# Kernel optimization log

Measured on AMD Instinct MI355X. Metric: run time of the kernel, lower is better.

## Reference

```python
import jax, jax.numpy as jnp
import numpy as np

N_NODES = 100000
N_EDGES = 1600000
IN_DIM = 256
OUT_DIM = 128


def setup_inputs() -> dict:
    key = jax.random.key(0)
    k1, k2, k3, k4, k5 = jax.random.split(key, 5)
    h = jax.random.normal(k1, (N_NODES, IN_DIM), dtype=jnp.float32)
    # xavier_normal-ish scales for the two weight matrices
    W = jax.random.normal(k2, (IN_DIM, OUT_DIM), dtype=jnp.float32) * (2.0 / np.sqrt(IN_DIM + OUT_DIM))
    a = jax.random.normal(k3, (2 * OUT_DIM,), dtype=jnp.float32) * (2.0 / np.sqrt(2 * OUT_DIM + 1))
    src = jax.random.randint(k4, (N_EDGES,), 0, N_NODES, dtype=jnp.int32)
    dst = jax.random.randint(k5, (N_EDGES,), 0, N_NODES, dtype=jnp.int32)
    return {"h": h, "W": W, "a": a, "src": src, "dst": dst}


def reference(h, W, a, src, dst):
    n = h.shape[0]
    d = W.shape[1]
    z = h @ W  # [N, out_dim]
    # attn_fc([z_src || z_dst]) == z_src @ a[:d] + z_dst @ a[d:]
    el = z @ a[:d]  # [N]
    er = z @ a[d:]  # [N]
    e = jax.nn.leaky_relu(el[src] + er[dst])  # [E], torch default slope 0.01
    # per-destination (segment) softmax, numerically stable
    seg_max = jax.ops.segment_max(e, dst, num_segments=n)
    e_exp = jnp.exp(e - seg_max[dst])
    denom = jax.ops.segment_sum(e_exp, dst, num_segments=n)
    alpha = e_exp / denom[dst]  # [E]
    # weighted scatter-sum of source z into destinations
    h_out = jax.ops.segment_sum(alpha[:, None] * z[src], dst, num_segments=n)
    return h_out
```

## Files before the change

### kernel.cpp

```cpp
#include <hip/hip_runtime.h>
#include <cstdint>
#include <cstddef>

#define N_NODES 100000
#define N_EDGES 1600000
#define IN_DIM  256
#define OUT_DIM 128

#define BSHIFT 7
#define BNODES 128
#define NBUCK  782
#define BCAP   3200
#define CNTMAX 2816
#define MAXE   6
#define EPB    2048
#define PB     782
#define GBP    1564

typedef __attribute__((ext_vector_type(8))) short bf16x8;
typedef __attribute__((ext_vector_type(4))) float f32x4;

__device__ __forceinline__ unsigned bf16rn(float f) {
    unsigned u = __float_as_uint(f);
    return (u + 0x7FFFu + ((u >> 16) & 1u)) >> 16;
}

__global__ __launch_bounds__(256) void setup_k(
    const float* __restrict__ W, unsigned short* __restrict__ w16s,
    int* __restrict__ bucket_cursor)
{
    int t = blockIdx.x * blockDim.x + threadIdx.x;
    if (t < NBUCK) bucket_cursor[t] = 0;
    if (t >= IN_DIM * OUT_DIM) return;
    int j  = t & 7;
    int n  = (t >> 3) & 15;
    int q  = (t >> 7) & 3;
    int c  = (t >> 9) & 7;
    int kc = t >> 12;
    int k   = kc * 32 + q * 8 + j;
    int dim = (c >> 1) * 32 + n * 2 + (c & 1);
    w16s[t] = (unsigned short)bf16rn(W[k * OUT_DIM + dim]);
}

__global__ __launch_bounds__(256, 3) void pg_k(
    const int* __restrict__ src, const int* __restrict__ dst,
    int* __restrict__ bucket_cursor, unsigned* __restrict__ ebuf,
    const float* __restrict__ h, const unsigned short* __restrict__ w16s,
    const float* __restrict__ a,
    unsigned short* __restrict__ z16, float* __restrict__ el, float* __restrict__ er)
{
    __shared__ int hist[NBUCK];
    __shared__ int gbaseL[NBUCK];
    const int t   = threadIdx.x;
    const int bid = blockIdx.x;

    if ((bid % 3) == 2) {
        const int pid = bid / 3;
        for (int i = t; i < NBUCK; i += 256) hist[i] = 0;
        __syncthreads();

        const int e0 = pid * EPB;
        int bucks[8], ranks[8];
        unsigned pk[8];
        #pragma unroll
        for (int k = 0; k < 8; ++k) {
            int e = e0 + k * 256 + t;
            bucks[k] = -1;
            if (e < N_EDGES) {
                int s = src[e], d = dst[e];
                int b = d >> BSHIFT;
                bucks[k] = b;
                ranks[k] = atomicAdd(&hist[b], 1);
                pk[k] = ((unsigned)s << BSHIFT) | (unsigned)(d & (BNODES - 1));
            }
        }
        __syncthreads();
        for (int i = t; i < NBUCK; i += 256) {
            int hc = hist[i];
            gbaseL[i] = hc ? atomicAdd(&bucket_cursor[i], hc) : 0;
        }
        __syncthreads();
        #pragma unroll
        for (int k = 0; k < 8; ++k)
            if (bucks[k] >= 0) {
                int p = gbaseL[bucks[k]] + ranks[k];
                if (p < BCAP)
                    ebuf[(size_t)bucks[k] * BCAP + p] = pk[k];
            }
        return;
    }

    const int gid  = (bid / 3) * 2 + (bid % 3);
    const int n0   = gid * 64;
    const int w    = t >> 6;
    const int lane = t & 63;
    const int q    = lane >> 4;
    const int col  = lane & 15;

    int row  = n0 + w * 16 + col;
    int lrow = (row < N_NODES) ? row : (N_NODES - 1);
    const float* hp = h + (size_t)lrow * IN_DIM + q * 8;

    float4 va[16];
    #pragma unroll
    for (int kc = 0; kc < 8; ++kc) {
        va[2 * kc]     = *(const float4*)(hp + kc * 32);
        va[2 * kc + 1] = *(const float4*)(hp + kc * 32 + 4);
    }

    f32x4 acc[8];
    #pragma unroll
    for (int c = 0; c < 8; ++c) acc[c] = (f32x4){0.f, 0.f, 0.f, 0.f};

    #pragma unroll
    for (int kc = 0; kc < 8; ++kc) {
        float4 v0 = va[2 * kc];
        float4 v1 = va[2 * kc + 1];
        bf16x8 af;
        af[0] = (short)bf16rn(v0.x); af[1] = (short)bf16rn(v0.y);
        af[2] = (short)bf16rn(v0.z); af[3] = (short)bf16rn(v0.w);
        af[4] = (short)bf16rn(v1.x); af[5] = (short)bf16rn(v1.y);
        af[6] = (short)bf16rn(v1.z); af[7] = (short)bf16rn(v1.w);
        #pragma unroll
        for (int c = 0; c < 8; ++c) {
            bf16x8 bfr = *(const bf16x8*)&w16s[((((kc * 8 + c) * 4 + q) * 16) + col) * 8];
            acc[c] = __builtin_amdgcn_mfma_f32_16x16x32_bf16(af, bfr, acc[c], 0, 0, 0);
        }
    }

    float aL[8], aR[8];
    #pragma unroll
    for (int c = 0; c < 8; ++c) {
        int dim = (c >> 1) * 32 + col * 2 + (c & 1);
        aL[c] = a[dim];
        aR[c] = a[128 + dim];
    }
    #pragma unroll
    for (int r = 0; r < 4; ++r) {
        int node = n0 + w * 16 + q * 4 + r;
        float sl = 0.f, sr = 0.f;
        #pragma unroll
        for (int c = 0; c < 8; ++c) {
            sl += acc[c][r] * aL[c];
            sr += acc[c][r] * aR[c];
        }
        #pragma unroll
        for (int o = 1; o < 16; o <<= 1) {
            sl += __shfl_xor(sl, o, 64);
            sr += __shfl_xor(sr, o, 64);
        }
        if (node < N_NODES) {
            #pragma unroll
            for (int g = 0; g < 4; ++g) {
                unsigned u = bf16rn(acc[2 * g][r]) | (bf16rn(acc[2 * g + 1][r]) << 16);
                ((unsigned*)z16)[(size_t)node * 64 + g * 16 + col] = u;
            }
            if (col == 0) { el[node] = sl; er[node] = sr; }
        }
    }
}

__global__ __launch_bounds__(512) void bn_k(
    const int* __restrict__ bucket_cursor, const unsigned* __restrict__ ebuf,
    const float* __restrict__ el, const float* __restrict__ er,
    const unsigned* __restrict__ z16, float* __restrict__ out)
{
    __shared__ float erL[BNODES];
    __shared__ int   deg[BNODES];
    __shared__ int   off[BNODES];
    __shared__ int   wvSum[2];
    __shared__ unsigned long long wsL[BCAP];

    const int b = blockIdx.x;
    const int t = threadIdx.x;
    int cnt = bucket_cursor[b];
    if (cnt > CNTMAX) cnt = CNTMAX;
    const unsigned* eb = ebuf + (size_t)b * BCAP;

    if (t < BNODES) {
        deg[t] = 0;
        int n = b * BNODES + t;
        erL[t] = (n < N_NODES) ? er[n] : 0.f;
    }
    __syncthreads();

    unsigned pv[MAXE]; int rk[MAXE]; float wv_[MAXE];
    #pragma unroll
    for (int k = 0; k < MAXE; ++k) {
        int i = t + k * 512;
        if (i < cnt) {
            unsigned v = eb[i];
            int s  = (int)(v >> BSHIFT);
            int ld = (int)(v & (BNODES - 1));
            float e = el[s] + erL[ld];
            e = (e > 0.0f) ? e : 0.01f * e;
            wv_[k] = __expf(e);
            rk[k]  = atomicAdd(&deg[ld], 1);
            pv[k]  = v;
        }
    }
    __syncthreads();

    int d = 0, pd = 0, incl = 0;
    if (t < BNODES) {
        d  = deg[t];
        pd = (d + 3) & ~3;
        incl = pd;
        #pragma unroll
        for (int o = 1; o < 64; o <<= 1) {
            int x = __shfl_up(incl, o, 64);
            if ((t & 63) >= o) incl += x;
        }
        if ((t & 63) == 63) wvSum[t >> 6] = incl;
    }
    __syncthreads();
    if (t < BNODES) off[t] = ((t >= 64) ? wvSum[0] : 0) + incl - pd;
    __syncthreads();

    #pragma unroll
    for (int k = 0; k < MAXE; ++k) {
        int i = t + k * 512;
        if (i < cnt) {
            int ld = (int)(pv[k] & (BNODES - 1));
            int p  = off[ld] + rk[k];
            wsL[p] = ((unsigned long long)__float_as_uint(wv_[k]) << 32)
                   | (pv[k] >> BSHIFT);
        }
    }
    if (t < BNODES) {
        int o = off[t];
        for (int j = o + d; j < o + pd; ++j) wsL[j] = 0ull;
    }
    __syncthreads();

    const int wv   = t >> 6;
    const int lane = t & 63;
    #pragma unroll 1
    for (int k = 0; k < BNODES / 8; ++k) {
        int ln = wv * (BNODES / 8) + k;
        int n  = b * BNODES + ln;
        if (n >= N_NODES) continue;
        int o   = off[ln];
        int dl  = deg[ln];
        int pdl = (dl + 3) & ~3;
        float acc0 = 0.f, acc1 = 0.f, dsum = 0.f;
        #pragma unroll 2
        for (int i = o; i < o + pdl; i += 4) {
            unsigned long long e0 = wsL[i],     e1 = wsL[i + 1];
            unsigned long long e2 = wsL[i + 2], e3 = wsL[i + 3];
            float w0 = __uint_as_float((unsigned)(e0 >> 32));
            float w1 = __uint_as_float((unsigned)(e1 >> 32));
            float w2 = __uint_as_float((unsigned)(e2 >> 32));
            float w3 = __uint_as_float((unsigned)(e3 >> 32));
            unsigned q0 = z16[(size_t)(unsigned)e0 * 64 + lane];
            unsigned q1 = z16[(size_t)(unsigned)e1 * 64 + lane];
            unsigned q2 = z16[(size_t)(unsigned)e2 * 64 + lane];
            unsigned q3 = z16[(size_t)(unsigned)e3 * 64 + lane];
            acc0 += w0 * __uint_as_float(q0 << 16)
                  + w1 * __uint_as_float(q1 << 16)
                  + w2 * __uint_as_float(q2 << 16)
                  + w3 * __uint_as_float(q3 << 16);
            acc1 += w0 * __uint_as_float(q0 & 0xFFFF0000u)
                  + w1 * __uint_as_float(q1 & 0xFFFF0000u)
                  + w2 * __uint_as_float(q2 & 0xFFFF0000u)
                  + w3 * __uint_as_float(q3 & 0xFFFF0000u);
            dsum += w0 + w1 + w2 + w3;
        }
        if (pdl > 0) {
            float inv = 1.0f / dsum;
            acc0 *= inv; acc1 *= inv;
        }
        *(float2*)&out[(size_t)n * OUT_DIM + lane * 2] = make_float2(acc0, acc1);
    }
}

extern "C" void kernel_launch(void* const* d_in, const int* in_sizes, int n_in,
                              void* d_out, int out_size, void* d_ws, size_t ws_size,
                              hipStream_t stream)
{
    (void)in_sizes; (void)n_in; (void)out_size; (void)ws_size;
    const float* h = (const float*)d_in[0];
    const float* W = (const float*)d_in[1];
    const float* a = (const float*)d_in[2];
    const int* src = (const int*)d_in[3];
    const int* dst = (const int*)d_in[4];
    float* out = (float*)d_out;

    char* ws = (char*)d_ws;
    size_t off = 0;
    auto alloc = [&](size_t bytes) -> char* {
        char* p = ws + off;
        off += (bytes + 255) & ~(size_t)255;
        return p;
    };
    unsigned short* z16  = (unsigned short*)alloc((size_t)N_NODES * OUT_DIM * 2);
    unsigned short* w16s = (unsigned short*)alloc((size_t)IN_DIM * OUT_DIM * 2);
    float*    el        = (float*)   alloc((size_t)N_NODES * 4);
    float*    er        = (float*)   alloc((size_t)N_NODES * 4);
    int*      bucket_cursor = (int*) alloc((size_t)NBUCK * 4);
    unsigned* ebuf      = (unsigned*)alloc((size_t)NBUCK * BCAP * 4);

    setup_k<<<(IN_DIM * OUT_DIM + 255) / 256, 256, 0, stream>>>(W, w16s, bucket_cursor);
    pg_k<<<PB + GBP, 256, 0, stream>>>(src, dst, bucket_cursor, ebuf,
                                       h, w16s, a, z16, el, er);
    bn_k<<<NBUCK, 512, 0, stream>>>(bucket_cursor, ebuf, el, er,
                                    (const unsigned*)z16, out);
}
```

Before: 288.1 us.

## Fuse edge partition and GEMM work into every block with alternating order

Before, the grid mixed dedicated partition blocks and GEMM blocks. Now every block does both a smaller edge-partition chunk and a 64-row GEMM tile, with odd blocks partitioning first and even blocks doing the GEMM first. The intent is to balance memory-bound and compute-bound phases inside each block and to interleave them across the GPU. The h loads are now issued inside the k-loop instead of being preloaded, and the occupancy hint is dropped from launch bounds, which may reduce memory-level parallelism.

Result: slower. 296.1 us (+2.8%).

```diff
diff --git a/kernel.cpp b/kernel.cpp
--- a/kernel.cpp
+++ b/kernel.cpp
@@ -13,9 +13,8 @@
 #define BCAP   3200
 #define CNTMAX 2816
 #define MAXE   6
-#define EPB    2048
-#define PB     782
-#define GBP    1564
+#define PEPB   1024
+#define PGB    1564
 
 typedef __attribute__((ext_vector_type(8))) short bf16x8;
 typedef __attribute__((ext_vector_type(4))) float f32x4;
@@ -42,56 +41,51 @@
     w16s[t] = (unsigned short)bf16rn(W[k * OUT_DIM + dim]);
 }
 
-__global__ __launch_bounds__(256, 3) void pg_k(
-    const int* __restrict__ src, const int* __restrict__ dst,
+__device__ __forceinline__ void do_partition(
+    int pid, int t, const int* __restrict__ src, const int* __restrict__ dst,
     int* __restrict__ bucket_cursor, unsigned* __restrict__ ebuf,
-    const float* __restrict__ h, const unsigned short* __restrict__ w16s,
-    const float* __restrict__ a,
-    unsigned short* __restrict__ z16, float* __restrict__ el, float* __restrict__ er)
-{
-    __shared__ int hist[NBUCK];
-    __shared__ int gbaseL[NBUCK];
-    const int t   = threadIdx.x;
-    const int bid = blockIdx.x;
-
-    if ((bid % 3) == 2) {
-        const int pid = bid / 3;
-        for (int i = t; i < NBUCK; i += 256) hist[i] = 0;
-        __syncthreads();
-
-        const int e0 = pid * EPB;
-        int bucks[8], ranks[8];
-        unsigned pk[8];
-        #pragma unroll
-        for (int k = 0; k < 8; ++k) {
-            int e = e0 + k * 256 + t;
-            bucks[k] = -1;
-            if (e < N_EDGES) {
-                int s = src[e], d = dst[e];
-                int b = d >> BSHIFT;
-                bucks[k] = b;
-                ranks[k] = atomicAdd(&hist[b], 1);
-                pk[k] = ((unsigned)s << BSHIFT) | (unsigned)(d & (BNODES - 1));
-            }
-        }
-        __syncthreads();
-        for (int i = t; i < NBUCK; i += 256) {
-            int hc = hist[i];
-            gbaseL[i] = hc ? atomicAdd(&bucket_cursor[i], hc) : 0;
-        }
-        __syncthreads();
-        #pragma unroll
-        for (int k = 0; k < 8; ++k)
-            if (bucks[k] >= 0) {
-                int p = gbaseL[bucks[k]] + ranks[k];
-                if (p < BCAP)
-                    ebuf[(size_t)bucks[k] * BCAP + p] = pk[k];
-            }
-        return;
-    }
-
-    const int gid  = (bid / 3) * 2 + (bid % 3);
+    int* hist, int* gbaseL)
+{
+    for (int i = t; i < NBUCK; i += 256) hist[i] = 0;
+    __syncthreads();
+
+    const int e0 = pid * PEPB;
+    int bucks[4], ranks[4];
+    unsigned pk[4];
+    #pragma unroll
+    for (int k = 0; k < 4; ++k) {
+        int e = e0 + k * 256 + t;
+        bucks[k] = -1;
+        if (e < N_EDGES) {
+            int s = src[e], d = dst[e];
+            int b = d >> BSHIFT;
+            bucks[k] = b;
+            ranks[k] = atomicAdd(&hist[b], 1);
+            pk[k] = ((unsigned)s << BSHIFT) | (unsigned)(d & (BNODES - 1));
+        }
+    }
+    __syncthreads();
+    for (int i = t; i < NBUCK; i += 256) {
+        int hc = hist[i];
+        gbaseL[i] = hc ? atomicAdd(&bucket_cursor[i], hc) : 0;
+    }
+    __syncthreads();
+    #pragma unroll
+    for (int k = 0; k < 4; ++k)
+        if (bucks[k] >= 0) {
+            int p = gbaseL[bucks[k]] + ranks[k];
+            if (p < BCAP)
+                ebuf[(size_t)bucks[k] * BCAP + p] = pk[k];
+        }
+}
+
+__device__ __forceinline__ void do_gemm(
+    int gid, int t, const float* __restrict__ h, const unsigned short* __restrict__ w16s,
+    const float* __restrict__ a, unsigned short* __restrict__ z16,
+    float* __restrict__ el, float* __restrict__ er)
+{
     const int n0   = gid * 64;
+    if (n0 >= N_NODES) return;
     const int w    = t >> 6;
     const int lane = t & 63;
     const int q    = lane >> 4;
@@ -101,21 +95,14 @@
     int lrow = (row < N_NODES) ? row : (N_NODES - 1);
     const float* hp = h + (size_t)lrow * IN_DIM + q * 8;
 
-    float4 va[16];
+    f32x4 acc[8];
+    #pragma unroll
+    for (int c = 0; c < 8; ++c) acc[c] = (f32x4){0.f, 0.f, 0.f, 0.f};
+
     #pragma unroll
     for (int kc = 0; kc < 8; ++kc) {
-        va[2 * kc]     = *(const float4*)(hp + kc * 32);
-        va[2 * kc + 1] = *(const float4*)(hp + kc * 32 + 4);
-    }
-
-    f32x4 acc[8];
-    #pragma unroll
-    for (int c = 0; c < 8; ++c) acc[c] = (f32x4){0.f, 0.f, 0.f, 0.f};
-
-    #pragma unroll
-    for (int kc = 0; kc < 8; ++kc) {
-        float4 v0 = va[2 * kc];
-        float4 v1 = va[2 * kc + 1];
+        float4 v0 = *(const float4*)(hp + kc * 32);
+        float4 v1 = *(const float4*)(hp + kc * 32 + 4);
         bf16x8 af;
         af[0] = (short)bf16rn(v0.x); af[1] = (short)bf16rn(v0.y);
         af[2] = (short)bf16rn(v0.z); af[3] = (short)bf16rn(v0.w);
@@ -157,6 +144,27 @@
             }
             if (col == 0) { el[node] = sl; er[node] = sr; }
         }
+    }
+}
+
+__global__ __launch_bounds__(256) void pg_k(
+    const int* __restrict__ src, const int* __restrict__ dst,
+    int* __restrict__ bucket_cursor, unsigned* __restrict__ ebuf,
+    const float* __restrict__ h, const unsigned short* __restrict__ w16s,
+    const float* __restrict__ a,
+    unsigned short* __restrict__ z16, float* __restrict__ el, float* __restrict__ er)
+{
+    __shared__ int hist[NBUCK];
+    __shared__ int gbaseL[NBUCK];
+    const int t   = threadIdx.x;
+    const int bid = blockIdx.x;
+
+    if (bid & 1) {
+        do_partition(bid, t, src, dst, bucket_cursor, ebuf, hist, gbaseL);
+        do_gemm(bid, t, h, w16s, a, z16, el, er);
+    } else {
+        do_gemm(bid, t, h, w16s, a, z16, el, er);
+        do_partition(bid, t, src, dst, bucket_cursor, ebuf, hist, gbaseL);
     }
 }
 
@@ -301,8 +309,8 @@
     unsigned* ebuf      = (unsigned*)alloc((size_t)NBUCK * BCAP * 4);
 
     setup_k<<<(IN_DIM * OUT_DIM + 255) / 256, 256, 0, stream>>>(W, w16s, bucket_cursor);
-    pg_k<<<PB + GBP, 256, 0, stream>>>(src, dst, bucket_cursor, ebuf,
-                                       h, w16s, a, z16, el, er);
+    pg_k<<<PGB, 256, 0, stream>>>(src, dst, bucket_cursor, ebuf,
+                                  h, w16s, a, z16, el, er);
     bn_k<<<NBUCK, 512, 0, stream>>>(bucket_cursor, ebuf, el, er,
                                     (const unsigned*)z16, out);
 }
```

## Halve bucket size and process two buckets per block with overlapped prep

Applied to the files above, without the earlier changes.

Shrinks destination buckets from 128 to 64 nodes and has each bn_k block handle two buckets. The second bucket's edge loads, exp weights and degree atomics are issued before the first bucket's gather loop, so their latency can hide behind it. Edge-list loads become vectorised uint4 reads and launch bounds request higher occupancy. pg_k drops the register prefetch of h rows and the partition grid is recomputed. This adds more shared memory per block and more bucket bookkeeping in the pre-pass.

New measurement: 287.6 us. No clear change (-0.2%).

```diff
diff --git a/kernel.cpp b/kernel.cpp
--- a/kernel.cpp
+++ b/kernel.cpp
@@ -7,15 +7,13 @@
 #define IN_DIM  256
 #define OUT_DIM 128
 
-#define BSHIFT 7
-#define BNODES 128
-#define NBUCK  782
-#define BCAP   3200
-#define CNTMAX 2816
-#define MAXE   6
+#define BSHIFT 6
+#define BNODES 64
+#define NBUCK  1563
+#define BCAP   1600
+#define CNTMAX 1408
 #define EPB    2048
-#define PB     782
-#define GBP    1564
+#define PGB    2346
 
 typedef __attribute__((ext_vector_type(8))) short bf16x8;
 typedef __attribute__((ext_vector_type(4))) float f32x4;
@@ -92,6 +90,7 @@
 
     const int gid  = (bid / 3) * 2 + (bid % 3);
     const int n0   = gid * 64;
+    if (n0 >= N_NODES) return;
     const int w    = t >> 6;
     const int lane = t & 63;
     const int q    = lane >> 4;
@@ -101,21 +100,14 @@
     int lrow = (row < N_NODES) ? row : (N_NODES - 1);
     const float* hp = h + (size_t)lrow * IN_DIM + q * 8;
 
-    float4 va[16];
+    f32x4 acc[8];
+    #pragma unroll
+    for (int c = 0; c < 8; ++c) acc[c] = (f32x4){0.f, 0.f, 0.f, 0.f};
+
     #pragma unroll
     for (int kc = 0; kc < 8; ++kc) {
-        va[2 * kc]     = *(const float4*)(hp + kc * 32);
-        va[2 * kc + 1] = *(const float4*)(hp + kc * 32 + 4);
-    }
-
-    f32x4 acc[8];
-    #pragma unroll
-    for (int c = 0; c < 8; ++c) acc[c] = (f32x4){0.f, 0.f, 0.f, 0.f};
-
-    #pragma unroll
-    for (int kc = 0; kc < 8; ++kc) {
-        float4 v0 = va[2 * kc];
-        float4 v1 = va[2 * kc + 1];
+        float4 v0 = *(const float4*)(hp + kc * 32);
+        float4 v1 = *(const float4*)(hp + kc * 32 + 4);
         bf16x8 af;
         af[0] = (short)bf16rn(v0.x); af[1] = (short)bf16rn(v0.y);
         af[2] = (short)bf16rn(v0.z); af[3] = (short)bf16rn(v0.w);
@@ -160,94 +152,121 @@
     }
 }
 
-__global__ __launch_bounds__(512) void bn_k(
+__global__ __launch_bounds__(512, 8) void bn_k(
     const int* __restrict__ bucket_cursor, const unsigned* __restrict__ ebuf,
     const float* __restrict__ el, const float* __restrict__ er,
     const unsigned* __restrict__ z16, float* __restrict__ out)
 {
-    __shared__ float erL[BNODES];
-    __shared__ int   deg[BNODES];
-    __shared__ int   off[BNODES];
-    __shared__ int   wvSum[2];
-    __shared__ unsigned long long wsL[BCAP];
-
-    const int b = blockIdx.x;
-    const int t = threadIdx.x;
-    int cnt = bucket_cursor[b];
-    if (cnt > CNTMAX) cnt = CNTMAX;
-    const unsigned* eb = ebuf + (size_t)b * BCAP;
+    __shared__ float erL[2 * BNODES];
+    __shared__ int   degA[BNODES], offA[BNODES];
+    __shared__ int   degB[BNODES], offB[BNODES];
+    __shared__ unsigned long long wsA[BCAP], wsB[BCAP];
+
+    const int blk = blockIdx.x;
+    const int t   = threadIdx.x;
+    const int bA  = blk * 2;
+    const int bB  = blk * 2 + 1;
+    const bool hasB = (bB < NBUCK);
+
+    int cA = bucket_cursor[bA]; if (cA > CNTMAX) cA = CNTMAX;
+    int cB = 0;
+    if (hasB) { cB = bucket_cursor[bB]; if (cB > CNTMAX) cB = CNTMAX; }
+
+    if (t < BNODES) { degA[t] = 0; degB[t] = 0; }
+    if (t < 2 * BNODES) {
+        int bucket = (t < BNODES) ? bA : bB;
+        int n = bucket * BNODES + (t & (BNODES - 1));
+        erL[t] = (bucket < NBUCK && n < N_NODES) ? er[n] : 0.f;
+    }
+    __syncthreads();
+
+    const int iA = 4 * t;
+    unsigned evsA[4] = {0u, 0u, 0u, 0u};
+    float wA[4]; int rkA[4];
+    if (iA < cA) {
+        uint4 v = *(const uint4*)&ebuf[(size_t)bA * BCAP + iA];
+        evsA[0] = v.x; evsA[1] = v.y; evsA[2] = v.z; evsA[3] = v.w;
+    }
+    {
+        float eg[4];
+        #pragma unroll
+        for (int j = 0; j < 4; ++j)
+            eg[j] = (iA + j < cA) ? el[evsA[j] >> BSHIFT] : 0.f;
+        #pragma unroll
+        for (int j = 0; j < 4; ++j) {
+            if (iA + j < cA) {
+                int ld = evsA[j] & (BNODES - 1);
+                float e = eg[j] + erL[ld];
+                e = (e > 0.f) ? e : 0.01f * e;
+                wA[j]  = __expf(e);
+                rkA[j] = atomicAdd(&degA[ld], 1);
+            }
+        }
+    }
+    __syncthreads();
 
     if (t < BNODES) {
-        deg[t] = 0;
-        int n = b * BNODES + t;
-        erL[t] = (n < N_NODES) ? er[n] : 0.f;
-    }
-    __syncthreads();
-
-    unsigned pv[MAXE]; int rk[MAXE]; float wv_[MAXE];
-    #pragma unroll
-    for (int k = 0; k < MAXE; ++k) {
-        int i = t + k * 512;
-        if (i < cnt) {
-            unsigned v = eb[i];
-            int s  = (int)(v >> BSHIFT);
-            int ld = (int)(v & (BNODES - 1));
-            float e = el[s] + erL[ld];
-            e = (e > 0.0f) ? e : 0.01f * e;
-            wv_[k] = __expf(e);
-            rk[k]  = atomicAdd(&deg[ld], 1);
-            pv[k]  = v;
-        }
-    }
-    __syncthreads();
-
-    int d = 0, pd = 0, incl = 0;
-    if (t < BNODES) {
-        d  = deg[t];
-        pd = (d + 3) & ~3;
-        incl = pd;
+        int d = degA[t], pd = (d + 3) & ~3, incl = pd;
         #pragma unroll
         for (int o = 1; o < 64; o <<= 1) {
             int x = __shfl_up(incl, o, 64);
-            if ((t & 63) >= o) incl += x;
-        }
-        if ((t & 63) == 63) wvSum[t >> 6] = incl;
-    }
-    __syncthreads();
-    if (t < BNODES) off[t] = ((t >= 64) ? wvSum[0] : 0) + incl - pd;
-    __syncthreads();
-
-    #pragma unroll
-    for (int k = 0; k < MAXE; ++k) {
-        int i = t + k * 512;
-        if (i < cnt) {
-            int ld = (int)(pv[k] & (BNODES - 1));
-            int p  = off[ld] + rk[k];
-            wsL[p] = ((unsigned long long)__float_as_uint(wv_[k]) << 32)
-                   | (pv[k] >> BSHIFT);
-        }
-    }
+            if (t >= o) incl += x;
+        }
+        offA[t] = incl - pd;
+    }
+    __syncthreads();
+
+    #pragma unroll
+    for (int j = 0; j < 4; ++j)
+        if (iA + j < cA) {
+            int ld = evsA[j] & (BNODES - 1);
+            wsA[offA[ld] + rkA[j]] =
+                ((unsigned long long)__float_as_uint(wA[j]) << 32) | (evsA[j] >> BSHIFT);
+        }
     if (t < BNODES) {
-        int o = off[t];
-        for (int j = o + d; j < o + pd; ++j) wsL[j] = 0ull;
-    }
-    __syncthreads();
+        int d = degA[t], pd = (d + 3) & ~3, o = offA[t];
+        for (int j = o + d; j < o + pd; ++j) wsA[j] = 0ull;
+    }
+    __syncthreads();
+
+    unsigned evsB[4] = {0u, 0u, 0u, 0u};
+    float wB[4]; int rkB[4];
+    if (iA < cB) {
+        uint4 v = *(const uint4*)&ebuf[(size_t)bB * BCAP + iA];
+        evsB[0] = v.x; evsB[1] = v.y; evsB[2] = v.z; evsB[3] = v.w;
+    }
+    {
+        float eg[4];
+        #pragma unroll
+        for (int j = 0; j < 4; ++j)
+            eg[j] = (iA + j < cB) ? el[evsB[j] >> BSHIFT] : 0.f;
+        #pragma unroll
+        for (int j = 0; j < 4; ++j) {
+            if (iA + j < cB) {
+                int ld = evsB[j] & (BNODES - 1);
+                float e = eg[j] + erL[BNODES + ld];
+                e = (e > 0.f) ? e : 0.01f * e;
+                wB[j]  = __expf(e);
+                rkB[j] = atomicAdd(&degB[ld], 1);
+            }
+        }
+    }
 
     const int wv   = t >> 6;
     const int lane = t & 63;
     #pragma unroll 1
     for (int k = 0; k < BNODES / 8; ++k) {
         int ln = wv * (BNODES / 8) + k;
-        int n  = b * BNODES + ln;
+        int n  = bA * BNODES + ln;
         if (n >= N_NODES) continue;
-        int o   = off[ln];
-        int dl  = deg[ln];
+        int o   = offA[ln];
+        int dl  = degA[ln];
         int pdl = (dl + 3) & ~3;
         float acc0 = 0.f, acc1 = 0.f, dsum = 0.f;
         #pragma unroll 2
         for (int i = o; i < o + pdl; i += 4) {
-            unsigned long long e0 = wsL[i],     e1 = wsL[i + 1];
-            unsigned long long e2 = wsL[i + 2], e3 = wsL[i + 3];
+            unsigned long long e0 = wsA[i],     e1 = wsA[i + 1];
+            unsigned long long e2 = wsA[i + 2], e3 = wsA[i + 3];
             float w0 = __uint_as_float((unsigned)(e0 >> 32));
             float w1 = __uint_as_float((unsigned)(e1 >> 32));
             float w2 = __uint_as_float((unsigned)(e2 >> 32));
@@ -272,6 +291,71 @@
         }
         *(float2*)&out[(size_t)n * OUT_DIM + lane * 2] = make_float2(acc0, acc1);
     }
+    __syncthreads();
+
+    if (t < BNODES) {
+        int d = degB[t], pd = (d + 3) & ~3, incl = pd;
+        #pragma unroll
+        for (int o = 1; o < 64; o <<= 1) {
+            int x = __shfl_up(incl, o, 64);
+            if (t >= o) incl += x;
+        }
+        offB[t] = incl - pd;
+    }
+    __syncthreads();
+
+    #pragma unroll
+    for (int j = 0; j < 4; ++j)
+        if (iA + j < cB) {
+            int ld = evsB[j] & (BNODES - 1);
+            wsB[offB[ld] + rkB[j]] =
+                ((unsigned long long)__float_as_uint(wB[j]) << 32) | (evsB[j] >> BSHIFT);
+        }
+    if (t < BNODES) {
+        int d = degB[t], pd = (d + 3) & ~3, o = offB[t];
+        for (int j = o + d; j < o + pd; ++j) wsB[j] = 0ull;
+    }
+    __syncthreads();
+
+    if (hasB) {
+        #pragma unroll 1
+        for (int k = 0; k < BNODES / 8; ++k) {
+            int ln = wv * (BNODES / 8) + k;
+            int n  = bB * BNODES + ln;
+            if (n >= N_NODES) continue;
+            int o   = offB[ln];
+            int dl  = degB[ln];
+            int pdl = (dl + 3) & ~3;
+            float acc0 = 0.f, acc1 = 0.f, dsum = 0.f;
+            #pragma unroll 2
+            for (int i = o; i < o + pdl; i += 4) {
+                unsigned long long e0 = wsB[i],     e1 = wsB[i + 1];
+                unsigned long long e2 = wsB[i + 2], e3 = wsB[i + 3];
+                float w0 = __uint_as_float((unsigned)(e0 >> 32));
+                float w1 = __uint_as_float((unsigned)(e1 >> 32));
+                float w2 = __uint_as_float((unsigned)(e2 >> 32));
+                float w3 = __uint_as_float((unsigned)(e3 >> 32));
+                unsigned q0 = z16[(size_t)(unsigned)e0 * 64 + lane];
+                unsigned q1 = z16[(size_t)(unsigned)e1 * 64 + lane];
+                unsigned q2 = z16[(size_t)(unsigned)e2 * 64 + lane];
+                unsigned q3 = z16[(size_t)(unsigned)e3 * 64 + lane];
+                acc0 += w0 * __uint_as_float(q0 << 16)
+                      + w1 * __uint_as_float(q1 << 16)
+                      + w2 * __uint_as_float(q2 << 16)
+                      + w3 * __uint_as_float(q3 << 16);
+                acc1 += w0 * __uint_as_float(q0 & 0xFFFF0000u)
+                      + w1 * __uint_as_float(q1 & 0xFFFF0000u)
+                      + w2 * __uint_as_float(q2 & 0xFFFF0000u)
+                      + w3 * __uint_as_float(q3 & 0xFFFF0000u);
+                dsum += w0 + w1 + w2 + w3;
+            }
+            if (pdl > 0) {
+                float inv = 1.0f / dsum;
+                acc0 *= inv; acc1 *= inv;
+            }
+            *(float2*)&out[(size_t)n * OUT_DIM + lane * 2] = make_float2(acc0, acc1);
+        }
+    }
 }
 
 extern "C" void kernel_launch(void* const* d_in, const int* in_sizes, int n_in,
@@ -301,8 +385,8 @@
     unsigned* ebuf      = (unsigned*)alloc((size_t)NBUCK * BCAP * 4);
 
     setup_k<<<(IN_DIM * OUT_DIM + 255) / 256, 256, 0, stream>>>(W, w16s, bucket_cursor);
-    pg_k<<<PB + GBP, 256, 0, stream>>>(src, dst, bucket_cursor, ebuf,
-                                       h, w16s, a, z16, el, er);
-    bn_k<<<NBUCK, 512, 0, stream>>>(bucket_cursor, ebuf, el, er,
-                                    (const unsigned*)z16, out);
-}
+    pg_k<<<PGB, 256, 0, stream>>>(src, dst, bucket_cursor, ebuf,
+                                  h, w16s, a, z16, el, er);
+    bn_k<<<(NBUCK + 1) / 2, 512, 0, stream>>>(bucket_cursor, ebuf, el, er,
+                                              (const unsigned*)z16, out);
+}
```

## Halve bucket size to 64 nodes and use 256-thread aggregation blocks

Applied to the files above, without the earlier changes.

Destination buckets shrink from 128 to 64 nodes, doubling the bucket count and halving per-block LDS staging. The aggregation kernel moves to 256 threads with a launch-bounds occupancy hint, and the prefix scan becomes a single wavefront scan. The GEMM part stops preloading all of h into registers and instead loads per k-chunk, and the combined grid is resized with an early exit. The aim is more resident blocks and better latency hiding, at the cost of more atomics on bucket cursors and smaller per-block work.

Measured after the change: 282.9 us. No clear change (-1.8%).

```diff
diff --git a/kernel.cpp b/kernel.cpp
--- a/kernel.cpp
+++ b/kernel.cpp
@@ -7,15 +7,14 @@
 #define IN_DIM  256
 #define OUT_DIM 128
 
-#define BSHIFT 7
-#define BNODES 128
-#define NBUCK  782
-#define BCAP   3200
-#define CNTMAX 2816
-#define MAXE   6
+#define BSHIFT 6
+#define BNODES 64
+#define NBUCK  1563
+#define BCAP   1600
+#define CNTMAX 1408
+#define MAXE   7
 #define EPB    2048
-#define PB     782
-#define GBP    1564
+#define PGB    2346
 
 typedef __attribute__((ext_vector_type(8))) short bf16x8;
 typedef __attribute__((ext_vector_type(4))) float f32x4;
@@ -92,6 +91,7 @@
 
     const int gid  = (bid / 3) * 2 + (bid % 3);
     const int n0   = gid * 64;
+    if (n0 >= N_NODES) return;
     const int w    = t >> 6;
     const int lane = t & 63;
     const int q    = lane >> 4;
@@ -101,21 +101,14 @@
     int lrow = (row < N_NODES) ? row : (N_NODES - 1);
     const float* hp = h + (size_t)lrow * IN_DIM + q * 8;
 
-    float4 va[16];
+    f32x4 acc[8];
+    #pragma unroll
+    for (int c = 0; c < 8; ++c) acc[c] = (f32x4){0.f, 0.f, 0.f, 0.f};
+
     #pragma unroll
     for (int kc = 0; kc < 8; ++kc) {
-        va[2 * kc]     = *(const float4*)(hp + kc * 32);
-        va[2 * kc + 1] = *(const float4*)(hp + kc * 32 + 4);
-    }
-
-    f32x4 acc[8];
-    #pragma unroll
-    for (int c = 0; c < 8; ++c) acc[c] = (f32x4){0.f, 0.f, 0.f, 0.f};
-
-    #pragma unroll
-    for (int kc = 0; kc < 8; ++kc) {
-        float4 v0 = va[2 * kc];
-        float4 v1 = va[2 * kc + 1];
+        float4 v0 = *(const float4*)(hp + kc * 32);
+        float4 v1 = *(const float4*)(hp + kc * 32 + 4);
         bf16x8 af;
         af[0] = (short)bf16rn(v0.x); af[1] = (short)bf16rn(v0.y);
         af[2] = (short)bf16rn(v0.z); af[3] = (short)bf16rn(v0.w);
@@ -160,7 +153,7 @@
     }
 }
 
-__global__ __launch_bounds__(512) void bn_k(
+__global__ __launch_bounds__(256, 8) void bn_k(
     const int* __restrict__ bucket_cursor, const unsigned* __restrict__ ebuf,
     const float* __restrict__ el, const float* __restrict__ er,
     const unsigned* __restrict__ z16, float* __restrict__ out)
@@ -168,8 +161,7 @@
     __shared__ float erL[BNODES];
     __shared__ int   deg[BNODES];
     __shared__ int   off[BNODES];
-    __shared__ int   wvSum[2];
-    __shared__ unsigned long long wsL[BCAP];
+    __shared__ unsigned long long ws[BCAP];
 
     const int b = blockIdx.x;
     const int t = threadIdx.x;
@@ -187,13 +179,13 @@
     unsigned pv[MAXE]; int rk[MAXE]; float wv_[MAXE];
     #pragma unroll
     for (int k = 0; k < MAXE; ++k) {
-        int i = t + k * 512;
+        int i = t + k * 256;
         if (i < cnt) {
             unsigned v = eb[i];
             int s  = (int)(v >> BSHIFT);
             int ld = (int)(v & (BNODES - 1));
             float e = el[s] + erL[ld];
-            e = (e > 0.0f) ? e : 0.01f * e;
+            e = (e > 0.f) ? e : 0.01f * e;
             wv_[k] = __expf(e);
             rk[k]  = atomicAdd(&deg[ld], 1);
             pv[k]  = v;
@@ -201,43 +193,38 @@
     }
     __syncthreads();
 
-    int d = 0, pd = 0, incl = 0;
     if (t < BNODES) {
-        d  = deg[t];
-        pd = (d + 3) & ~3;
-        incl = pd;
+        int d = deg[t], pd = (d + 3) & ~3, incl = pd;
         #pragma unroll
         for (int o = 1; o < 64; o <<= 1) {
             int x = __shfl_up(incl, o, 64);
-            if ((t & 63) >= o) incl += x;
-        }
-        if ((t & 63) == 63) wvSum[t >> 6] = incl;
-    }
-    __syncthreads();
-    if (t < BNODES) off[t] = ((t >= 64) ? wvSum[0] : 0) + incl - pd;
+            if (t >= o) incl += x;
+        }
+        off[t] = incl - pd;
+    }
     __syncthreads();
 
     #pragma unroll
     for (int k = 0; k < MAXE; ++k) {
-        int i = t + k * 512;
+        int i = t + k * 256;
         if (i < cnt) {
             int ld = (int)(pv[k] & (BNODES - 1));
-            int p  = off[ld] + rk[k];
-            wsL[p] = ((unsigned long long)__float_as_uint(wv_[k]) << 32)
-                   | (pv[k] >> BSHIFT);
+            ws[off[ld] + rk[k]] =
+                ((unsigned long long)__float_as_uint(wv_[k]) << 32)
+                | (pv[k] >> BSHIFT);
         }
     }
     if (t < BNODES) {
-        int o = off[t];
-        for (int j = o + d; j < o + pd; ++j) wsL[j] = 0ull;
+        int d = deg[t], pd = (d + 3) & ~3, o = off[t];
+        for (int j = o + d; j < o + pd; ++j) ws[j] = 0ull;
     }
     __syncthreads();
 
     const int wv   = t >> 6;
     const int lane = t & 63;
     #pragma unroll 1
-    for (int k = 0; k < BNODES / 8; ++k) {
-        int ln = wv * (BNODES / 8) + k;
+    for (int k = 0; k < BNODES / 4; ++k) {
+        int ln = wv * (BNODES / 4) + k;
         int n  = b * BNODES + ln;
         if (n >= N_NODES) continue;
         int o   = off[ln];
@@ -246,8 +233,8 @@
         float acc0 = 0.f, acc1 = 0.f, dsum = 0.f;
         #pragma unroll 2
         for (int i = o; i < o + pdl; i += 4) {
-            unsigned long long e0 = wsL[i],     e1 = wsL[i + 1];
-            unsigned long long e2 = wsL[i + 2], e3 = wsL[i + 3];
+            unsigned long long e0 = ws[i],     e1 = ws[i + 1];
+            unsigned long long e2 = ws[i + 2], e3 = ws[i + 3];
             float w0 = __uint_as_float((unsigned)(e0 >> 32));
             float w1 = __uint_as_float((unsigned)(e1 >> 32));
             float w2 = __uint_as_float((unsigned)(e2 >> 32));
@@ -301,8 +288,8 @@
     unsigned* ebuf      = (unsigned*)alloc((size_t)NBUCK * BCAP * 4);
 
     setup_k<<<(IN_DIM * OUT_DIM + 255) / 256, 256, 0, stream>>>(W, w16s, bucket_cursor);
-    pg_k<<<PB + GBP, 256, 0, stream>>>(src, dst, bucket_cursor, ebuf,
-                                       h, w16s, a, z16, el, er);
-    bn_k<<<NBUCK, 512, 0, stream>>>(bucket_cursor, ebuf, el, er,
+    pg_k<<<PGB, 256, 0, stream>>>(src, dst, bucket_cursor, ebuf,
+                                  h, w16s, a, z16, el, er);
+    bn_k<<<NBUCK, 256, 0, stream>>>(bucket_cursor, ebuf, el, er,
                                     (const unsigned*)z16, out);
 }
```
